# Kernel optimization log

Measured on AMD Instinct MI355X. Metric: run time of the kernel, lower is better.

The kernel has to match this reference:

```python
import jax, jax.numpy as jnp
import numpy as np

NEG = 9e15

def adj_helper(adj):
    n = adj.shape[0]
    a = adj + jnp.eye(n, dtype=adj.dtype)
    d1 = jnp.sqrt(a.sum(axis=-1))[:, None]
    d2 = jnp.sqrt(a.sum(axis=0))[None, :]
    return a / d1 / d2

def gcn(adj, x, Ws):
    a = adj_helper(adj)
    z = x
    for W in Ws:
        z = jax.nn.elu(a @ (z @ W))
    return z

def sage(adj, x, layers):
    deg = jnp.clip(adj.sum(axis=-1, keepdims=True), 1e-5, None)
    a = adj / deg
    z = x
    for (Wp, b, W) in layers:
        h = jax.nn.elu(z @ Wp + b)
        h = a @ h
        z = jax.nn.elu(jnp.concatenate([z, h], axis=1) @ W)
    return z

def sim_graph_cos(h, k):
    n = h.shape[0]
    length = jnp.sqrt(jnp.sum(h * h, axis=-1))          # [n]
    sim = (h @ h.T) / (length[:, None] * length[None, :])
    sim = sim - jnp.eye(n, dtype=sim.dtype) * NEG        # mask self
    val, ids = jax.lax.top_k(sim, k)                     # [n,k]
    rows = jnp.arange(n)[:, None]
    return jnp.zeros_like(sim).at[rows, ids].set(val)

def setup_inputs() -> dict:
    key = jax.random.key(0)
    ks = jax.random.split(key, 16)
    N, F, H, E, K = 6144, 128, 128, 16384, 32
    s = 0.05
    adj = (jax.random.uniform(ks[0], (N, N)) < 0.002).astype(jnp.float32)
    x = jax.random.normal(ks[1], (N, F), dtype=jnp.float32)
    src = jax.random.randint(ks[2], (E,), 0, N)
    dst = jax.random.randint(ks[3], (E,), 0, N)
    labels = (jax.random.uniform(ks[4], (E,)) < 0.5).astype(jnp.float32)
    return {
        "src": src, "dst": dst, "labels": labels, "adj": adj, "x": x,
        "Wg1": jax.random.normal(ks[5], (F, H)) * s,
        "Wg2": jax.random.normal(ks[6], (H, H)) * s,
        "Wp1": jax.random.normal(ks[7], (F, H)) * s,
        "b1": jax.random.normal(ks[8], (1, H)) * s,
        "Ws1": jax.random.normal(ks[9], (F + H, H)) * s,
        "Wp2": jax.random.normal(ks[10], (H, H)) * s,
        "b2": jax.random.normal(ks[11], (1, H)) * s,
        "Ws2": jax.random.normal(ks[12], (H + H, H)) * s,
        "PredW": jax.random.normal(ks[13], (2 * H, 2 * H)) * s,
        "PredB": jax.random.normal(ks[14], (1, 1)) * s,
        "top_k": 32,
    }

def reference(src, dst, labels, adj, x, Wg1, Wg2, Wp1, b1, Ws1, Wp2, b2, Ws2, PredW, PredB, top_k):
    h1 = gcn(adj, x, [Wg1, Wg2])                 # [N,H]
    sim_adj = sim_graph_cos(x, top_k)            # [N,N] top-k sparse (dense-stored)
    h2 = sage(sim_adj, x, [(Wp1, b1, Ws1), (Wp2, b2, Ws2)])  # [N,H]
    h = jnp.concatenate([h1, h2], axis=1)        # [N,2H]
    src_h = h[src]                               # [E,2H]
    dst_h = h[dst]                               # [E,2H]
    logits = jnp.einsum('ed,df,ef->e', src_h, PredW, dst_h) + PredB[0, 0]
    # BCEWithLogitsLoss (mean, numerically stable)
    loss = jnp.mean(jnp.maximum(logits, 0) - logits * labels
                    + jnp.log1p(jnp.exp(-jnp.abs(logits))))
    return loss, logits
```

## Files before the change

kernel.cpp:

```cpp
#include <hip/hip_runtime.h>
#include <hip/hip_bf16.h>
#include <stdint.h>

#define N_NODES 6144
#define FDIM    128
#define EEDGES  16384
#define KTOP    32
#define KSEL    48
#define MAXNBR  64
#define MAXCAND 512
#define NTILES  96
#define GRIDY   16
#define TPB     (NTILES/GRIDY)

typedef short bf16x8 __attribute__((ext_vector_type(8)));
typedef float f32x4  __attribute__((ext_vector_type(4)));

__device__ __forceinline__ float elu_f(float x){ return x > 0.f ? x : expm1f(x); }

__device__ __forceinline__ unsigned short f2bf(float f){
  unsigned int u = __float_as_uint(f);
  u += 0x7FFFu + ((u >> 16) & 1u);
  return (unsigned short)(u >> 16);
}
__device__ __forceinline__ float bf2f(unsigned short h){
  return __uint_as_float(((unsigned int)h) << 16);
}

__global__ __launch_bounds__(256) void prep(const float* __restrict__ adj,
    const float* __restrict__ x, int* __restrict__ nbr, int* __restrict__ nbrcnt,
    int* __restrict__ colcnt, unsigned short* __restrict__ xbf,
    float* __restrict__ xninv, float* __restrict__ cat1){
  const int b = blockIdx.x, t = threadIdx.x;
  if (b < N_NODES){
    const int i = b;
    __shared__ int s_cnt;
    if (t == 0) s_cnt = 0;
    __syncthreads();
    const float4* row = (const float4*)(adj + (size_t)i * N_NODES);
    for (int v = t; v < N_NODES/4; v += 256){
      float4 f = row[v];
      int c = v * 4;
      if (f.x != 0.f){ int s = atomicAdd(&s_cnt,1); if (s < MAXNBR) nbr[i*MAXNBR+s] = c;   atomicAdd(&colcnt[c],1); }
      if (f.y != 0.f){ int s = atomicAdd(&s_cnt,1); if (s < MAXNBR) nbr[i*MAXNBR+s] = c+1; atomicAdd(&colcnt[c+1],1); }
      if (f.z != 0.f){ int s = atomicAdd(&s_cnt,1); if (s < MAXNBR) nbr[i*MAXNBR+s] = c+2; atomicAdd(&colcnt[c+2],1); }
      if (f.w != 0.f){ int s = atomicAdd(&s_cnt,1); if (s < MAXNBR) nbr[i*MAXNBR+s] = c+3; atomicAdd(&colcnt[c+3],1); }
    }
    __syncthreads();
    if (t == 0) nbrcnt[i] = min(s_cnt, MAXNBR);
  } else {
    const int i = (b - N_NODES)*2 + (t >> 7);
    const int tl = t & 127;
    float v = x[(size_t)i*FDIM + tl];
    xbf[(size_t)i*FDIM + tl] = f2bf(v);
    cat1[(size_t)i*256 + tl] = v;
    float s = v * v;
    for (int o = 32; o > 0; o >>= 1) s += __shfl_down(s, o, 64);
    __shared__ float ws[4];
    if ((t & 63) == 0) ws[t >> 6] = s;
    __syncthreads();
    if (tl == 0) xninv[i] = rsqrtf(ws[(t>>7)*2] + ws[(t>>7)*2 + 1]);
  }
}

__global__ __launch_bounds__(256) void simgemm(const unsigned short* __restrict__ xbf,
    const float* __restrict__ xninv, unsigned short* __restrict__ sim,
    float* __restrict__ gmax){
  const int t    = threadIdx.x;
  const int R0   = blockIdx.x * 64;
  const int tb0  = blockIdx.y * TPB;
  const int lane = t & 63, w = t >> 6;
  const int lr   = lane & 15, q8 = (lane >> 4) * 8, quad = lane >> 4;

  __shared__ unsigned short Abf[64][136];
  __shared__ unsigned short Bbf[64][136];
  __shared__ unsigned short Stile[64][72];
  __shared__ float nrow[64];
  __shared__ float ncol[64];
  __shared__ float wmax[4][64];

  for (int e = t; e < 64*16; e += 256){
    int r = e >> 4, c8 = e & 15;
    *(uint4*)&Abf[r][c8*8] = ((const uint4*)(xbf + (size_t)(R0 + r)*FDIM))[c8];
  }
  if (t < 64) nrow[t] = xninv[R0 + t];

  for (int tb = tb0; tb < tb0 + TPB; ++tb){
    __syncthreads();
    for (int e = t; e < 64*16; e += 256){
      int r = e >> 4, c8 = e & 15;
      *(uint4*)&Bbf[r][c8*8] = ((const uint4*)(xbf + (size_t)(tb*64 + r)*FDIM))[c8];
    }
    if (t < 64) ncol[t] = xninv[tb*64 + t];
    __syncthreads();

    f32x4 acc[4] = {};
#pragma unroll
    for (int kb = 0; kb < 4; ++kb){
      bf16x8 bcol = *(const bf16x8*)&Bbf[w*16 + lr][kb*32 + q8];
#pragma unroll
      for (int f = 0; f < 4; ++f){
        bf16x8 arow = *(const bf16x8*)&Abf[f*16 + lr][kb*32 + q8];
        acc[f] = __builtin_amdgcn_mfma_f32_16x16x32_bf16(bcol, arow, acc[f], 0, 0, 0);
      }
    }
    const int scol0 = w*16 + quad*4;
    const float nc0 = ncol[scol0], nc1 = ncol[scol0+1],
                nc2 = ncol[scol0+2], nc3 = ncol[scol0+3];
#pragma unroll
    for (int f = 0; f < 4; ++f){
      const int srow = f*16 + lr;
      const float nr = nrow[srow];
      const int grow = R0 + srow, gcol0 = tb*64 + scol0;
      float v0 = acc[f][0]*nr*nc0, v1 = acc[f][1]*nr*nc1,
            v2 = acc[f][2]*nr*nc2, v3 = acc[f][3]*nr*nc3;
      if (grow == gcol0    ) v0 = -2.0f;
      if (grow == gcol0 + 1) v1 = -2.0f;
      if (grow == gcol0 + 2) v2 = -2.0f;
      if (grow == gcol0 + 3) v3 = -2.0f;
      unsigned int h0 = f2bf(v0), h1 = f2bf(v1), h2 = f2bf(v2), h3 = f2bf(v3);
      uint2 p; p.x = h0 | (h1 << 16); p.y = h2 | (h3 << 16);
      *(uint2*)&Stile[srow][scol0] = p;
      float rmax = fmaxf(fmaxf(bf2f(h0), bf2f(h1)), fmaxf(bf2f(h2), bf2f(h3)));
      rmax = fmaxf(rmax, __shfl_xor(rmax, 16, 64));
      rmax = fmaxf(rmax, __shfl_xor(rmax, 32, 64));
      if (quad == 0) wmax[w][srow] = rmax;
    }
    __syncthreads();
#pragma unroll
    for (int e0 = 0; e0 < 2; ++e0){
      int e = t + e0*256;
      int r = e >> 3, c8 = e & 7;
      *(uint4*)&sim[(size_t)(R0 + r)*N_NODES + tb*64 + c8*8] = *(uint4*)&Stile[r][c8*8];
    }
    if (t < 64){
      float g = fmaxf(fmaxf(wmax[0][t], wmax[1][t]), fmaxf(wmax[2][t], wmax[3][t]));
      gmax[(size_t)(R0 + t)*NTILES + tb] = g;
    }
  }
}

__global__ __launch_bounds__(256) void refine_scan(const float* __restrict__ x,
    const float* __restrict__ xninv, const unsigned short* __restrict__ sim,
    const float* __restrict__ gmax, float* __restrict__ tval, int* __restrict__ tidx,
    float* __restrict__ deginv){
  const int i = blockIdx.x, t = threadIdx.x;
  __shared__ float xi[128];
  __shared__ float gm[NTILES];
  __shared__ float tauv;
  __shared__ float cv[MAXCAND];
  __shared__ int   ci[MAXCAND];
  __shared__ float sel[KTOP];
  __shared__ int   cnt;
  if (t == 0) cnt = 0;
  if (t < 32) *(float4*)&xi[t*4] = *(const float4*)(x + (size_t)i*FDIM + t*4);
  if (t < NTILES) gm[t] = gmax[(size_t)i*NTILES + t];
  __syncthreads();
  if (t < NTILES){
    float v = gm[t]; int rank = 0;
    for (int j = 0; j < NTILES; ++j){
      float u = gm[j];
      if (u > v || (u == v && j < t)) rank++;
    }
    if (rank == KSEL-1) tauv = v;
  }
  __syncthreads();
  const float taui = tauv;
  const uint4* srow = (const uint4*)(sim + (size_t)i*N_NODES);
  for (int v8 = t; v8 < N_NODES/8; v8 += 256){
    uint4 u = srow[v8];
    const unsigned short* h = (const unsigned short*)&u;
#pragma unroll
    for (int q = 0; q < 8; ++q){
      if (bf2f(h[q]) >= taui){
        int s = atomicAdd(&cnt, 1);
        if (s < MAXCAND) ci[s] = v8*8 + q;
      }
    }
  }
  __syncthreads();
  int n = cnt; if (n > MAXCAND) n = MAXCAND;
  const float ni = xninv[i];
  const int part = t & 3, cb = t >> 2;
  for (int c0 = 0; c0 < n; c0 += 64){
    const int c = c0 + cb;
    float acc = 0.f;
    int idx = 0;
    if (c < n){
      idx = ci[c];
      const float* xc = x + (size_t)idx*FDIM + part*32;
#pragma unroll
      for (int q = 0; q < 8; ++q){
        float4 f = *(const float4*)(xc + q*4);
        const float* a = &xi[part*32 + q*4];
        acc += a[0]*f.x + a[1]*f.y + a[2]*f.z + a[3]*f.w;
      }
    }
    acc += __shfl_xor(acc, 1, 64);
    acc += __shfl_xor(acc, 2, 64);
    if (c < n && part == 0) cv[c] = acc * ni * xninv[idx];
  }
  __syncthreads();
  for (int c = t; c < n; c += 256){
    float v = cv[c]; int id = ci[c];
    int rank = 0;
    for (int j = 0; j < n; ++j){
      float u = cv[j];
      if (u > v || (u == v && ci[j] < id)) rank++;
    }
    if (rank < KTOP){
      tval[(size_t)i*KTOP + rank] = v;
      tidx[(size_t)i*KTOP + rank] = id;
      sel[rank] = v;
    }
  }
  __syncthreads();
  if (t == 0){
    float s = 0.f;
    for (int q = 0; q < KTOP; ++q) s += sel[q];
    deginv[i] = 1.0f / fmaxf(s, 1e-5f);
  }
}

__device__ __forceinline__ void gemm_body(const float* __restrict__ A, int lda,
    const float* __restrict__ B, int ldb, const float* __restrict__ bias,
    float* __restrict__ C, int ldc, int K, int act, int R0, int C0){
  const int t = threadIdx.x;
  const int rg = t >> 4, cg = t & 15;
  __shared__ float Alds[32][34];
  __shared__ float Blds[32][68];
  float4 acc0 = {0,0,0,0}, acc1 = {0,0,0,0};
  for (int kc = 0; kc < K; kc += 32){
    __syncthreads();
    { int r = t >> 3, k0 = (t & 7) * 4;
      float4 f = *(const float4*)(A + (size_t)(R0 + r)*lda + kc + k0);
      Alds[k0+0][r] = f.x; Alds[k0+1][r] = f.y; Alds[k0+2][r] = f.z; Alds[k0+3][r] = f.w; }
#pragma unroll
    for (int e = 0; e < 2; ++e){
      int idx = t + e*256;
      int k = idx >> 4, m4 = idx & 15;
      *(float4*)&Blds[k][m4*4] = *(const float4*)(B + (size_t)(kc + k)*ldb + C0 + m4*4);
    }
    __syncthreads();
#pragma unroll
    for (int k = 0; k < 32; ++k){
      float2 a = *(const float2*)&Alds[k][rg*2];
      float4 b = *(const float4*)&Blds[k][cg*4];
      acc0.x += a.x*b.x; acc0.y += a.x*b.y; acc0.z += a.x*b.z; acc0.w += a.x*b.w;
      acc1.x += a.y*b.x; acc1.y += a.y*b.y; acc1.z += a.y*b.z; acc1.w += a.y*b.w;
    }
  }
  const int r0 = R0 + rg*2, c0 = C0 + cg*4;
  float4 bb = {0,0,0,0};
  if (bias) bb = *(const float4*)&bias[c0];
  acc0.x += bb.x; acc0.y += bb.y; acc0.z += bb.z; acc0.w += bb.w;
  acc1.x += bb.x; acc1.y += bb.y; acc1.z += bb.z; acc1.w += bb.w;
  if (act){
    acc0.x = elu_f(acc0.x); acc0.y = elu_f(acc0.y); acc0.z = elu_f(acc0.z); acc0.w = elu_f(acc0.w);
    acc1.x = elu_f(acc1.x); acc1.y = elu_f(acc1.y); acc1.z = elu_f(acc1.z); acc1.w = elu_f(acc1.w);
  }
  *(float4*)&C[(size_t)r0*ldc + c0] = acc0;
  *(float4*)&C[(size_t)(r0+1)*ldc + c0] = acc1;
}

__global__ __launch_bounds__(256) void gemm_dual(const float* __restrict__ A,
    const float* __restrict__ B1, const float* __restrict__ B2,
    const float* __restrict__ bias2, float* __restrict__ C1, float* __restrict__ C2,
    const int* __restrict__ nbrcnt, const int* __restrict__ colcnt,
    float* __restrict__ d1inv, float* __restrict__ d2inv){
  const int t = threadIdx.x;
  const int R0 = blockIdx.x * 32, C0 = blockIdx.y * 64;
  if (blockIdx.y == 0 && t < 32){
    int i = R0 + t;
    d1inv[i] = rsqrtf((float)(nbrcnt[i] + 1));
    d2inv[i] = rsqrtf((float)(colcnt[i] + 1));
  }
  const int rg = t >> 4, cg = t & 15;
  __shared__ float Alds[32][34];
  __shared__ float B1lds[32][68];
  __shared__ float B2lds[32][68];
  float4 p0 = {0,0,0,0}, p1 = {0,0,0,0};
  float4 q0 = {0,0,0,0}, q1 = {0,0,0,0};
  for (int kc = 0; kc < FDIM; kc += 32){
    __syncthreads();
    { int r = t >> 3, k0 = (t & 7) * 4;
      float4 f = *(const float4*)(A + (size_t)(R0 + r)*FDIM + kc + k0);
      Alds[k0+0][r] = f.x; Alds[k0+1][r] = f.y; Alds[k0+2][r] = f.z; Alds[k0+3][r] = f.w; }
#pragma unroll
    for (int e = 0; e < 2; ++e){
      int idx = t + e*256;
      int k = idx >> 4, m4 = idx & 15;
      *(float4*)&B1lds[k][m4*4] = *(const float4*)(B1 + (size_t)(kc + k)*FDIM + C0 + m4*4);
      *(float4*)&B2lds[k][m4*4] = *(const float4*)(B2 + (size_t)(kc + k)*FDIM + C0 + m4*4);
    }
    __syncthreads();
#pragma unroll
    for (int k = 0; k < 32; ++k){
      float2 a = *(const float2*)&Alds[k][rg*2];
      float4 b = *(const float4*)&B1lds[k][cg*4];
      float4 c = *(const float4*)&B2lds[k][cg*4];
      p0.x += a.x*b.x; p0.y += a.x*b.y; p0.z += a.x*b.z; p0.w += a.x*b.w;
      p1.x += a.y*b.x; p1.y += a.y*b.y; p1.z += a.y*b.z; p1.w += a.y*b.w;
      q0.x += a.x*c.x; q0.y += a.x*c.y; q0.z += a.x*c.z; q0.w += a.x*c.w;
      q1.x += a.y*c.x; q1.y += a.y*c.y; q1.z += a.y*c.z; q1.w += a.y*c.w;
    }
  }
  const int r0 = R0 + rg*2, c0 = C0 + cg*4;
  *(float4*)&C1[(size_t)r0*FDIM + c0] = p0;
  *(float4*)&C1[(size_t)(r0+1)*FDIM + c0] = p1;
  float4 bb = *(const float4*)&bias2[c0];
  q0.x = elu_f(q0.x + bb.x); q0.y = elu_f(q0.y + bb.y); q0.z = elu_f(q0.z + bb.z); q0.w = elu_f(q0.w + bb.w);
  q1.x = elu_f(q1.x + bb.x); q1.y = elu_f(q1.y + bb.y); q1.z = elu_f(q1.z + bb.z); q1.w = elu_f(q1.w + bb.w);
  *(float4*)&C2[(size_t)r0*FDIM + c0] = q0;
  *(float4*)&C2[(size_t)(r0+1)*FDIM + c0] = q1;
}

template<int M>
__global__ __launch_bounds__(256) void gemm_k(const float* __restrict__ A, int lda,
    const float* __restrict__ B, const float* __restrict__ bias,
    float* __restrict__ C, int ldc, int K, int act){
  gemm_body(A, lda, B, M, bias, C, ldc, K, act, blockIdx.x*32, blockIdx.y*64);
}

__global__ __launch_bounds__(128) void spmm_pair(const float* __restrict__ T1,
    const int* __restrict__ nbr, const int* __restrict__ nbrcnt,
    const float* __restrict__ d1inv, const float* __restrict__ d2inv,
    float* __restrict__ z1,
    const float* __restrict__ T2, const float* __restrict__ tval,
    const int* __restrict__ tidx, const float* __restrict__ deginv,
    float* __restrict__ cat1r){
  const int b = blockIdx.x, t = threadIdx.x;
  if (b < N_NODES){
    const int i = b;
    float acc = T1[(size_t)i*FDIM + t] * d2inv[i];
    const int cnt = nbrcnt[i];
    const int* nb = nbr + (size_t)i*MAXNBR;
    for (int s = 0; s < cnt; ++s){
      int j = nb[s];
      acc += T1[(size_t)j*FDIM + t] * d2inv[j];
    }
    z1[(size_t)i*FDIM + t] = elu_f(acc * d1inv[i]);
  } else {
    const int i = b - N_NODES;
    float acc = 0.f;
    const float* vv = tval + (size_t)i*KTOP;
    const int*   ii = tidx + (size_t)i*KTOP;
    for (int s = 0; s < KTOP; ++s)
      acc += vv[s] * T2[(size_t)ii[s]*FDIM + t];
    cat1r[(size_t)i*256 + t] = acc * deginv[i];
  }
}

__global__ __launch_bounds__(256) void dual_stage1(const float* __restrict__ z1,
    const float* __restrict__ Wg2, float* __restrict__ T1,
    const float* __restrict__ cat1, const float* __restrict__ Ws1,
    float* __restrict__ cat2){
  const int b = blockIdx.x;
  if (b < 384){
    gemm_body(z1, FDIM, Wg2, FDIM, nullptr, T1, FDIM, FDIM, 0,
              (b % 192)*32, (b / 192)*64);
  } else {
    const int bb = b - 384;
    gemm_body(cat1, 256, Ws1, FDIM, nullptr, cat2, 256, 256, 1,
              (bb % 192)*32, (bb / 192)*64);
  }
}

__global__ __launch_bounds__(256) void dual_stage2(const float* __restrict__ T1,
    const int* __restrict__ nbr, const int* __restrict__ nbrcnt,
    const float* __restrict__ d1inv, const float* __restrict__ d2inv,
    float* __restrict__ hcat,
    const float* __restrict__ cat2, const float* __restrict__ Wp2,
    const float* __restrict__ b2, float* __restrict__ T2){
  const int b = blockIdx.x, t = threadIdx.x;
  if (b < 3072){
    const int i = b*2 + (t >> 7);
    const int tl = t & 127;
    float acc = T1[(size_t)i*FDIM + tl] * d2inv[i];
    const int cnt = nbrcnt[i];
    const int* nb = nbr + (size_t)i*MAXNBR;
    for (int s = 0; s < cnt; ++s){
      int j = nb[s];
      acc += T1[(size_t)j*FDIM + tl] * d2inv[j];
    }
    hcat[(size_t)i*256 + tl] = elu_f(acc * d1inv[i]);
  } else {
    const int bb = b - 3072;
    gemm_body(cat2, 256, Wp2, FDIM, b2, T2, FDIM, FDIM, 1,
              (bb % 192)*32, (bb / 192)*64);
  }
}

__global__ __launch_bounds__(128) void spmm_sage(const float* __restrict__ P,
    const float* __restrict__ tval, const int* __restrict__ tidx,
    const float* __restrict__ deginv, float* __restrict__ C, int ldc){
  const int i = blockIdx.x, t = threadIdx.x;
  float acc = 0.f;
  const float* vv = tval + (size_t)i*KTOP;
  const int*   ii = tidx + (size_t)i*KTOP;
  for (int s = 0; s < KTOP; ++s)
    acc += vv[s] * P[(size_t)ii[s]*FDIM + t];
  C[(size_t)i*ldc + t] = acc * deginv[i];
}

__global__ __launch_bounds__(256) void edge_loss(const int* __restrict__ src,
    const int* __restrict__ dst, const float* __restrict__ labels,
    const float* __restrict__ HP, const float* __restrict__ hcat,
    const float* __restrict__ predB, float* __restrict__ out,
    float* __restrict__ partial){
  const int t = threadIdx.x;
  const int e = blockIdx.x*4 + (t >> 6);
  const int lane = t & 63;
  const int s = src[e], d = dst[e];
  const float* hp = HP   + (size_t)s*256;
  const float* hc = hcat + (size_t)d*256;
  float acc = 0.f;
  for (int k = lane; k < 256; k += 64) acc += hp[k] * hc[k];
  for (int o = 32; o > 0; o >>= 1) acc += __shfl_down(acc, o, 64);
  __shared__ float terms[4];
  if (lane == 0){
    float l = acc + predB[0];
    out[1 + e] = l;
    float y = labels[e];
    terms[t >> 6] = fmaxf(l, 0.f) - l*y + log1pf(expf(-fabsf(l)));
  }
  __syncthreads();
  if (t == 0) partial[blockIdx.x] = terms[0] + terms[1] + terms[2] + terms[3];
}

__global__ __launch_bounds__(256) void reduce_loss(const float* __restrict__ partial,
    float* __restrict__ out){
  const int t = threadIdx.x, lane = t & 63, w = t >> 6;
  float s = 0.f;
  for (int i = t; i < EEDGES/4; i += 256) s += partial[i];
  for (int o = 32; o > 0; o >>= 1) s += __shfl_down(s, o, 64);
  __shared__ float ws[4];
  if (lane == 0) ws[w] = s;
  __syncthreads();
  if (t == 0) out[0] = (ws[0] + ws[1] + ws[2] + ws[3]) * (1.0f / EEDGES);
}

extern "C" void kernel_launch(void* const* d_in, const int* in_sizes, int n_in,
                              void* d_out, int out_size, void* d_ws, size_t ws_size,
                              hipStream_t stream){
  (void)in_sizes; (void)n_in; (void)out_size; (void)ws_size;
  const int*   src    = (const int*)d_in[0];
  const int*   dst    = (const int*)d_in[1];
  const float* labels = (const float*)d_in[2];
  const float* adj    = (const float*)d_in[3];
  const float* x      = (const float*)d_in[4];
  const float* Wg1    = (const float*)d_in[5];
  const float* Wg2    = (const float*)d_in[6];
  const float* Wp1    = (const float*)d_in[7];
  const float* b1     = (const float*)d_in[8];
  const float* Ws1    = (const float*)d_in[9];
  const float* Wp2    = (const float*)d_in[10];
  const float* b2     = (const float*)d_in[11];
  const float* Ws2    = (const float*)d_in[12];
  const float* PredW  = (const float*)d_in[13];
  const float* PredB  = (const float*)d_in[14];

  char* ws = (char*)d_ws;
  size_t off = 0;
  auto alloc = [&](size_t bytes)->void*{
    void* p = ws + off; off += (bytes + 255) & ~(size_t)255; return p; };

  int*   colcnt = (int*)  alloc((size_t)N_NODES*4);
  int*   nbrcnt = (int*)  alloc((size_t)N_NODES*4);
  int*   nbr    = (int*)  alloc((size_t)N_NODES*MAXNBR*4);
  float* d1inv  = (float*)alloc((size_t)N_NODES*4);
  float* d2inv  = (float*)alloc((size_t)N_NODES*4);
  float* xninv  = (float*)alloc((size_t)N_NODES*4);
  unsigned short* xbf = (unsigned short*)alloc((size_t)N_NODES*FDIM*2);
  float* tval   = (float*)alloc((size_t)N_NODES*KTOP*4);
  int*   tidx   = (int*)  alloc((size_t)N_NODES*KTOP*4);
  float* dginv  = (float*)alloc((size_t)N_NODES*4);
  float* gmax   = (float*)alloc((size_t)N_NODES*NTILES*4);
  float* partial= (float*)alloc((size_t)(EEDGES/4)*4);
  float* T1     = (float*)alloc((size_t)N_NODES*FDIM*4);
  float* T2     = (float*)alloc((size_t)N_NODES*FDIM*4);
  float* z1     = (float*)alloc((size_t)N_NODES*FDIM*4);
  float* cat1   = (float*)alloc((size_t)N_NODES*256*4);
  float* cat2   = (float*)alloc((size_t)N_NODES*256*4);
  float* hcat   = (float*)alloc((size_t)N_NODES*256*4);
  unsigned short* sim = (unsigned short*)alloc((size_t)N_NODES*N_NODES*2);
  float* out    = (float*)d_out;

  hipMemsetAsync(colcnt, 0, (size_t)N_NODES*4, stream);

  prep       <<<N_NODES + N_NODES/2, 256, 0, stream>>>(adj, x, nbr, nbrcnt, colcnt, xbf, xninv, cat1);
  simgemm    <<<dim3(N_NODES/64, GRIDY), 256, 0, stream>>>(xbf, xninv, sim, gmax);
  refine_scan<<<N_NODES, 256, 0, stream>>>(x, xninv, sim, gmax, tval, tidx, dginv);

  gemm_dual  <<<dim3(N_NODES/32, 2), 256, 0, stream>>>(x, Wg1, Wp1, b1, T1, T2,
                                                       nbrcnt, colcnt, d1inv, d2inv);
  spmm_pair  <<<2*N_NODES, 128, 0, stream>>>(T1, nbr, nbrcnt, d1inv, d2inv, z1,
                                             T2, tval, tidx, dginv, cat1 + 128);
  dual_stage1<<<768, 256, 0, stream>>>(z1, Wg2, T1, cat1, Ws1, cat2);
  dual_stage2<<<3072 + 384, 256, 0, stream>>>(T1, nbr, nbrcnt, d1inv, d2inv, hcat,
                                              cat2, Wp2, b2, T2);
  spmm_sage  <<<N_NODES, 128, 0, stream>>>(T2, tval, tidx, dginv, cat2 + 128, 256);
  gemm_k<128><<<dim3(N_NODES/32, 2), 256, 0, stream>>>(cat2, 256, Ws2, nullptr, hcat + 128, 256, 256, 1);

  gemm_k<256><<<dim3(N_NODES/32, 4), 256, 0, stream>>>(hcat, 256, PredW, nullptr, cat1, 256, 256, 0);
  edge_loss  <<<EEDGES/4, 256, 0, stream>>>(src, dst, labels, cat1, hcat, PredB, out, partial);
  reduce_loss<<<1, 256, 0, stream>>>(partial, out);
}
```

Measured before the change: 471.2 us.

## Quantize similarity matrix to 8-bit codes and fuse dense GEMM into refine kernel

The candidate-filter similarity matrix and the per-tile maxima are stored as 8-bit codes instead of bf16 and float. This halves the N×N intermediate traffic in both the write and the scan phases. The exact top-k is still refined from fp32 dot products of the candidates, and self-indices are now excluded explicitly rather than through the masked value. The separate gemm_dual launch is merged into refine_dual as extra blocks, removing one launch and letting the two run concurrently. Coarser quantization can admit more candidates per row, which risks overflowing MAXCAND and dropping true neighbours.

After: 495.6 us. 1.05x slower.

```diff
diff --git a/kernel.cpp b/kernel.cpp
--- a/kernel.cpp
+++ b/kernel.cpp
@@ -23,8 +23,9 @@
   u += 0x7FFFu + ((u >> 16) & 1u);
   return (unsigned short)(u >> 16);
 }
-__device__ __forceinline__ float bf2f(unsigned short h){
-  return __uint_as_float(((unsigned int)h) << 16);
+__device__ __forceinline__ int vcode(float v){
+  int c = (int)((v + 1.0f)*127.5f + 0.5f);
+  return c < 0 ? 0 : (c > 255 ? 255 : c);
 }
 
 __global__ __launch_bounds__(256) void prep(const float* __restrict__ adj,
@@ -64,8 +65,8 @@
 }
 
 __global__ __launch_bounds__(256) void simgemm(const unsigned short* __restrict__ xbf,
-    const float* __restrict__ xninv, unsigned short* __restrict__ sim,
-    float* __restrict__ gmax){
+    const float* __restrict__ xninv, unsigned char* __restrict__ sim8,
+    unsigned char* __restrict__ gmax8){
   const int t    = threadIdx.x;
   const int R0   = blockIdx.x * 64;
   const int tb0  = blockIdx.y * TPB;
@@ -74,10 +75,10 @@
 
   __shared__ unsigned short Abf[64][136];
   __shared__ unsigned short Bbf[64][136];
-  __shared__ unsigned short Stile[64][72];
+  __shared__ unsigned int   Stile32[64*20];
   __shared__ float nrow[64];
   __shared__ float ncol[64];
-  __shared__ float wmax[4][64];
+  __shared__ int   wmaxI[4][64];
 
   for (int e = t; e < 64*16; e += 256){
     int r = e >> 4, c8 = e & 15;
@@ -118,63 +119,125 @@
       if (grow == gcol0 + 1) v1 = -2.0f;
       if (grow == gcol0 + 2) v2 = -2.0f;
       if (grow == gcol0 + 3) v3 = -2.0f;
-      unsigned int h0 = f2bf(v0), h1 = f2bf(v1), h2 = f2bf(v2), h3 = f2bf(v3);
-      uint2 p; p.x = h0 | (h1 << 16); p.y = h2 | (h3 << 16);
-      *(uint2*)&Stile[srow][scol0] = p;
-      float rmax = fmaxf(fmaxf(bf2f(h0), bf2f(h1)), fmaxf(bf2f(h2), bf2f(h3)));
-      rmax = fmaxf(rmax, __shfl_xor(rmax, 16, 64));
-      rmax = fmaxf(rmax, __shfl_xor(rmax, 32, 64));
-      if (quad == 0) wmax[w][srow] = rmax;
-    }
-    __syncthreads();
-#pragma unroll
-    for (int e0 = 0; e0 < 2; ++e0){
-      int e = t + e0*256;
-      int r = e >> 3, c8 = e & 7;
-      *(uint4*)&sim[(size_t)(R0 + r)*N_NODES + tb*64 + c8*8] = *(uint4*)&Stile[r][c8*8];
+      int c0 = vcode(v0), c1 = vcode(v1), c2 = vcode(v2), c3 = vcode(v3);
+      Stile32[srow*20 + w*4 + quad] =
+        (unsigned)c0 | ((unsigned)c1 << 8) | ((unsigned)c2 << 16) | ((unsigned)c3 << 24);
+      int rmax = max(max(c0, c1), max(c2, c3));
+      rmax = max(rmax, __shfl_xor(rmax, 16, 64));
+      rmax = max(rmax, __shfl_xor(rmax, 32, 64));
+      if (quad == 0) wmaxI[w][srow] = rmax;
+    }
+    __syncthreads();
+    {
+      int r = t >> 2, c4 = (t & 3)*4;
+      *(uint4*)&sim8[(size_t)(R0 + r)*N_NODES + tb*64 + (t & 3)*16] = *(uint4*)&Stile32[r*20 + c4];
     }
     if (t < 64){
-      float g = fmaxf(fmaxf(wmax[0][t], wmax[1][t]), fmaxf(wmax[2][t], wmax[3][t]));
-      gmax[(size_t)(R0 + t)*NTILES + tb] = g;
-    }
-  }
-}
-
-__global__ __launch_bounds__(256) void refine_scan(const float* __restrict__ x,
-    const float* __restrict__ xninv, const unsigned short* __restrict__ sim,
-    const float* __restrict__ gmax, float* __restrict__ tval, int* __restrict__ tidx,
-    float* __restrict__ deginv){
-  const int i = blockIdx.x, t = threadIdx.x;
+      int g = max(max(wmaxI[0][t], wmaxI[1][t]), max(wmaxI[2][t], wmaxI[3][t]));
+      gmax8[(size_t)(R0 + t)*NTILES + tb] = (unsigned char)g;
+    }
+  }
+}
+
+__device__ __forceinline__ void gemm_dual_body(const float* __restrict__ A,
+    const float* __restrict__ B1, const float* __restrict__ B2,
+    const float* __restrict__ bias2, float* __restrict__ C1, float* __restrict__ C2,
+    int R0, int C0){
+  const int t = threadIdx.x;
+  const int rg = t >> 4, cg = t & 15;
+  __shared__ float Alds[32][34];
+  __shared__ float B1lds[32][68];
+  __shared__ float B2lds[32][68];
+  float4 p0 = {0,0,0,0}, p1 = {0,0,0,0};
+  float4 q0 = {0,0,0,0}, q1 = {0,0,0,0};
+  for (int kc = 0; kc < FDIM; kc += 32){
+    __syncthreads();
+    { int r = t >> 3, k0 = (t & 7) * 4;
+      float4 f = *(const float4*)(A + (size_t)(R0 + r)*FDIM + kc + k0);
+      Alds[k0+0][r] = f.x; Alds[k0+1][r] = f.y; Alds[k0+2][r] = f.z; Alds[k0+3][r] = f.w; }
+#pragma unroll
+    for (int e = 0; e < 2; ++e){
+      int idx = t + e*256;
+      int k = idx >> 4, m4 = idx & 15;
+      *(float4*)&B1lds[k][m4*4] = *(const float4*)(B1 + (size_t)(kc + k)*FDIM + C0 + m4*4);
+      *(float4*)&B2lds[k][m4*4] = *(const float4*)(B2 + (size_t)(kc + k)*FDIM + C0 + m4*4);
+    }
+    __syncthreads();
+#pragma unroll
+    for (int k = 0; k < 32; ++k){
+      float2 a = *(const float2*)&Alds[k][rg*2];
+      float4 b = *(const float4*)&B1lds[k][cg*4];
+      float4 c = *(const float4*)&B2lds[k][cg*4];
+      p0.x += a.x*b.x; p0.y += a.x*b.y; p0.z += a.x*b.z; p0.w += a.x*b.w;
+      p1.x += a.y*b.x; p1.y += a.y*b.y; p1.z += a.y*b.z; p1.w += a.y*b.w;
+      q0.x += a.x*c.x; q0.y += a.x*c.y; q0.z += a.x*c.z; q0.w += a.x*c.w;
+      q1.x += a.y*c.x; q1.y += a.y*c.y; q1.z += a.y*c.z; q1.w += a.y*c.w;
+    }
+  }
+  const int r0 = R0 + rg*2, c0 = C0 + cg*4;
+  *(float4*)&C1[(size_t)r0*FDIM + c0] = p0;
+  *(float4*)&C1[(size_t)(r0+1)*FDIM + c0] = p1;
+  float4 bb = *(const float4*)&bias2[c0];
+  q0.x = elu_f(q0.x + bb.x); q0.y = elu_f(q0.y + bb.y); q0.z = elu_f(q0.z + bb.z); q0.w = elu_f(q0.w + bb.w);
+  q1.x = elu_f(q1.x + bb.x); q1.y = elu_f(q1.y + bb.y); q1.z = elu_f(q1.z + bb.z); q1.w = elu_f(q1.w + bb.w);
+  *(float4*)&C2[(size_t)r0*FDIM + c0] = q0;
+  *(float4*)&C2[(size_t)(r0+1)*FDIM + c0] = q1;
+}
+
+__global__ __launch_bounds__(256) void refine_dual(const float* __restrict__ x,
+    const float* __restrict__ xninv, const unsigned char* __restrict__ sim8,
+    const unsigned char* __restrict__ gmax8, float* __restrict__ tval,
+    int* __restrict__ tidx, float* __restrict__ deginv,
+    const float* __restrict__ Wg1, const float* __restrict__ Wp1,
+    const float* __restrict__ b1, float* __restrict__ T1, float* __restrict__ T2,
+    const int* __restrict__ nbrcnt, const int* __restrict__ colcnt,
+    float* __restrict__ d1inv, float* __restrict__ d2inv){
+  const int t = threadIdx.x;
+  if (blockIdx.x >= N_NODES){
+    const int bb = blockIdx.x - N_NODES;
+    const int R0 = (bb % 192)*32, C0 = (bb / 192)*64;
+    if (bb < 192 && t < 32){
+      int i = R0 + t;
+      d1inv[i] = rsqrtf((float)(nbrcnt[i] + 1));
+      d2inv[i] = rsqrtf((float)(colcnt[i] + 1));
+    }
+    gemm_dual_body(x, Wg1, Wp1, b1, T1, T2, R0, C0);
+    return;
+  }
+  const int i = blockIdx.x;
   __shared__ float xi[128];
-  __shared__ float gm[NTILES];
-  __shared__ float tauv;
+  __shared__ int   gm[NTILES];
+  __shared__ int   tauc;
   __shared__ float cv[MAXCAND];
   __shared__ int   ci[MAXCAND];
   __shared__ float sel[KTOP];
   __shared__ int   cnt;
   if (t == 0) cnt = 0;
   if (t < 32) *(float4*)&xi[t*4] = *(const float4*)(x + (size_t)i*FDIM + t*4);
-  if (t < NTILES) gm[t] = gmax[(size_t)i*NTILES + t];
+  if (t < NTILES) gm[t] = gmax8[(size_t)i*NTILES + t];
   __syncthreads();
   if (t < NTILES){
-    float v = gm[t]; int rank = 0;
+    int v = gm[t], rank = 0;
     for (int j = 0; j < NTILES; ++j){
-      float u = gm[j];
+      int u = gm[j];
       if (u > v || (u == v && j < t)) rank++;
     }
-    if (rank == KSEL-1) tauv = v;
-  }
-  __syncthreads();
-  const float taui = tauv;
-  const uint4* srow = (const uint4*)(sim + (size_t)i*N_NODES);
-  for (int v8 = t; v8 < N_NODES/8; v8 += 256){
-    uint4 u = srow[v8];
-    const unsigned short* h = (const unsigned short*)&u;
-#pragma unroll
-    for (int q = 0; q < 8; ++q){
-      if (bf2f(h[q]) >= taui){
-        int s = atomicAdd(&cnt, 1);
-        if (s < MAXCAND) ci[s] = v8*8 + q;
+    if (rank == KSEL-1) tauc = v;
+  }
+  __syncthreads();
+  const int tc = tauc;
+  const uint4* srow = (const uint4*)(sim8 + (size_t)i*N_NODES);
+  for (int v16 = t; v16 < N_NODES/16; v16 += 256){
+    uint4 u = srow[v16];
+    const unsigned char* hb = (const unsigned char*)&u;
+#pragma unroll
+    for (int q = 0; q < 16; ++q){
+      if ((int)hb[q] >= tc){
+        int idx = v16*16 + q;
+        if (idx != i){
+          int s = atomicAdd(&cnt, 1);
+          if (s < MAXCAND) ci[s] = idx;
+        }
       }
     }
   }
@@ -261,58 +324,6 @@
   }
   *(float4*)&C[(size_t)r0*ldc + c0] = acc0;
   *(float4*)&C[(size_t)(r0+1)*ldc + c0] = acc1;
-}
-
-__global__ __launch_bounds__(256) void gemm_dual(const float* __restrict__ A,
-    const float* __restrict__ B1, const float* __restrict__ B2,
-    const float* __restrict__ bias2, float* __restrict__ C1, float* __restrict__ C2,
-    const int* __restrict__ nbrcnt, const int* __restrict__ colcnt,
-    float* __restrict__ d1inv, float* __restrict__ d2inv){
-  const int t = threadIdx.x;
-  const int R0 = blockIdx.x * 32, C0 = blockIdx.y * 64;
-  if (blockIdx.y == 0 && t < 32){
-    int i = R0 + t;
-    d1inv[i] = rsqrtf((float)(nbrcnt[i] + 1));
-    d2inv[i] = rsqrtf((float)(colcnt[i] + 1));
-  }
-  const int rg = t >> 4, cg = t & 15;
-  __shared__ float Alds[32][34];
-  __shared__ float B1lds[32][68];
-  __shared__ float B2lds[32][68];
-  float4 p0 = {0,0,0,0}, p1 = {0,0,0,0};
-  float4 q0 = {0,0,0,0}, q1 = {0,0,0,0};
-  for (int kc = 0; kc < FDIM; kc += 32){
-    __syncthreads();
-    { int r = t >> 3, k0 = (t & 7) * 4;
-      float4 f = *(const float4*)(A + (size_t)(R0 + r)*FDIM + kc + k0);
-      Alds[k0+0][r] = f.x; Alds[k0+1][r] = f.y; Alds[k0+2][r] = f.z; Alds[k0+3][r] = f.w; }
-#pragma unroll
-    for (int e = 0; e < 2; ++e){
-      int idx = t + e*256;
-      int k = idx >> 4, m4 = idx & 15;
-      *(float4*)&B1lds[k][m4*4] = *(const float4*)(B1 + (size_t)(kc + k)*FDIM + C0 + m4*4);
-      *(float4*)&B2lds[k][m4*4] = *(const float4*)(B2 + (size_t)(kc + k)*FDIM + C0 + m4*4);
-    }
-    __syncthreads();
-#pragma unroll
-    for (int k = 0; k < 32; ++k){
-      float2 a = *(const float2*)&Alds[k][rg*2];
-      float4 b = *(const float4*)&B1lds[k][cg*4];
-      float4 c = *(const float4*)&B2lds[k][cg*4];
-      p0.x += a.x*b.x; p0.y += a.x*b.y; p0.z += a.x*b.z; p0.w += a.x*b.w;
-      p1.x += a.y*b.x; p1.y += a.y*b.y; p1.z += a.y*b.z; p1.w += a.y*b.w;
-      q0.x += a.x*c.x; q0.y += a.x*c.y; q0.z += a.x*c.z; q0.w += a.x*c.w;
-      q1.x += a.y*c.x; q1.y += a.y*c.y; q1.z += a.y*c.z; q1.w += a.y*c.w;
-    }
-  }
-  const int r0 = R0 + rg*2, c0 = C0 + cg*4;
-  *(float4*)&C1[(size_t)r0*FDIM + c0] = p0;
-  *(float4*)&C1[(size_t)(r0+1)*FDIM + c0] = p1;
-  float4 bb = *(const float4*)&bias2[c0];
-  q0.x = elu_f(q0.x + bb.x); q0.y = elu_f(q0.y + bb.y); q0.z = elu_f(q0.z + bb.z); q0.w = elu_f(q0.w + bb.w);
-  q1.x = elu_f(q1.x + bb.x); q1.y = elu_f(q1.y + bb.y); q1.z = elu_f(q1.z + bb.z); q1.w = elu_f(q1.w + bb.w);
-  *(float4*)&C2[(size_t)r0*FDIM + c0] = q0;
-  *(float4*)&C2[(size_t)(r0+1)*FDIM + c0] = q1;
 }
 
 template<int M>
@@ -475,7 +486,7 @@
   float* tval   = (float*)alloc((size_t)N_NODES*KTOP*4);
   int*   tidx   = (int*)  alloc((size_t)N_NODES*KTOP*4);
   float* dginv  = (float*)alloc((size_t)N_NODES*4);
-  float* gmax   = (float*)alloc((size_t)N_NODES*NTILES*4);
+  unsigned char* gmax8 = (unsigned char*)alloc((size_t)N_NODES*NTILES);
   float* partial= (float*)alloc((size_t)(EEDGES/4)*4);
   float* T1     = (float*)alloc((size_t)N_NODES*FDIM*4);
   float* T2     = (float*)alloc((size_t)N_NODES*FDIM*4);
@@ -483,17 +494,16 @@
   float* cat1   = (float*)alloc((size_t)N_NODES*256*4);
   float* cat2   = (float*)alloc((size_t)N_NODES*256*4);
   float* hcat   = (float*)alloc((size_t)N_NODES*256*4);
-  unsigned short* sim = (unsigned short*)alloc((size_t)N_NODES*N_NODES*2);
+  unsigned char* sim8 = (unsigned char*)alloc((size_t)N_NODES*N_NODES);
   float* out    = (float*)d_out;
 
   hipMemsetAsync(colcnt, 0, (size_t)N_NODES*4, stream);
 
   prep       <<<N_NODES + N_NODES/2, 256, 0, stream>>>(adj, x, nbr, nbrcnt, colcnt, xbf, xninv, cat1);
-  simgemm    <<<dim3(N_NODES/64, GRIDY), 256, 0, stream>>>(xbf, xninv, sim, gmax);
-  refine_scan<<<N_NODES, 256, 0, stream>>>(x, xninv, sim, gmax, tval, tidx, dginv);
-
-  gemm_dual  <<<dim3(N_NODES/32, 2), 256, 0, stream>>>(x, Wg1, Wp1, b1, T1, T2,
-                                                       nbrcnt, colcnt, d1inv, d2inv);
+  simgemm    <<<dim3(N_NODES/64, GRIDY), 256, 0, stream>>>(xbf, xninv, sim8, gmax8);
+  refine_dual<<<N_NODES + 384, 256, 0, stream>>>(x, xninv, sim8, gmax8, tval, tidx, dginv,
+                                                 Wg1, Wp1, b1, T1, T2,
+                                                 nbrcnt, colcnt, d1inv, d2inv);
   spmm_pair  <<<2*N_NODES, 128, 0, stream>>>(T1, nbr, nbrcnt, d1inv, d2inv, z1,
                                              T2, tval, tidx, dginv, cat1 + 128);
   dual_stage1<<<768, 256, 0, stream>>>(z1, Wg2, T1, cat1, Ws1, cat2);
```
